# Kernel optimization log

Hardware: AMD Instinct MI355X
Metric: run time of the kernel (lower is better)

## Reference

```python
import jax, jax.numpy as jnp
import numpy as np

TAU = 0.07          # temperature
NEG = -1.0e9        # mask fill value (matches torch masked_fill)
EPS = 1e-12         # F.normalize eps

B1 = 4096
B2 = 4096
FDIM = 128


def setup_inputs() -> dict:
    key = jax.random.key(0)
    k1, k2 = jax.random.split(key)
    return {
        "feat_cls1": jax.random.normal(k1, (B1, FDIM), dtype=jnp.float32),
        "feat_cls2": jax.random.normal(k2, (B2, FDIM), dtype=jnp.float32),
    }


def reference(feat_cls1, feat_cls2):
    # concat both classes -> [B, F]
    feats = jnp.concatenate([feat_cls1, feat_cls2], axis=0)
    # F.normalize(dim=1): x / max(||x||, eps)
    norm = jnp.maximum(jnp.linalg.norm(feats, axis=1, keepdims=True), EPS)
    feats = feats / norm

    B = feats.shape[0]
    # similarity matrix [B, B]
    sim = (feats @ feats.T) / TAU

    labels = jnp.concatenate([
        jnp.zeros((feat_cls1.shape[0],), dtype=jnp.int32),
        jnp.ones((feat_cls2.shape[0],), dtype=jnp.int32),
    ])
    same_cls = labels[:, None] == labels[None, :]          # [B, B] bool
    eye = jnp.eye(B, dtype=bool)
    pool = same_cls & ~eye                                 # same-class, not self

    # select_mode == 'nearest': positive = same-class neighbor with max sim
    # (every row has >=1 same-class non-self entry since B1,B2 >= 2)
    pos_idx = jnp.argmax(jnp.where(pool, sim, NEG), axis=1)  # [B] int

    # allowed logits: all other-class entries + the single chosen positive; no diagonal
    pos_onehot = jax.nn.one_hot(pos_idx, B, dtype=bool)
    allow = (~same_cls) | pos_onehot
    allow = allow & ~eye

    sim_masked = jnp.where(allow, sim, NEG)
    # cross-entropy with target = pos_idx, mean over all B rows (all valid here)
    logz = jax.nn.logsumexp(sim_masked, axis=1)                              # [B]
    pos_logit = jnp.take_along_axis(sim_masked, pos_idx[:, None], axis=1)[:, 0]
    loss = jnp.mean(logz - pos_logit)
    return loss
```

## Files before the change

kernel.cpp:

```cpp
#include <hip/hip_runtime.h>
#include <math.h>
#include <stdint.h>

#define NB1   4096
#define NBTOT 8192
#define NFD   128
#define ECOLS 1024
#define BROWS 128
#define BCOLS 128
#define NTILES (ECOLS / BCOLS)

typedef __attribute__((ext_vector_type(8))) _Float16 f16x8;
typedef __attribute__((ext_vector_type(4))) float f32x4;
typedef _Float16 f16;

__device__ __forceinline__ void gl16(const f16* g, char* l) {
    __builtin_amdgcn_global_load_lds(
        (const __attribute__((address_space(1))) unsigned int*)g,
        (__attribute__((address_space(3))) unsigned int*)l,
        16, 0, 0);
}

__global__ void norm_k(const float* __restrict__ f1, const float* __restrict__ f2,
                       f16* __restrict__ nfh) {
    const int w = threadIdx.x >> 6, lane = threadIdx.x & 63;
    const int row = blockIdx.x * 4 + w;
    const float* src = (row < NB1) ? (f1 + (size_t)row * NFD)
                                   : (f2 + (size_t)(row - NB1) * NFD);
    const float2 v = *reinterpret_cast<const float2*>(src + 2 * lane);
    float s = v.x * v.x + v.y * v.y;
#pragma unroll
    for (int m = 32; m >= 1; m >>= 1) s += __shfl_xor(s, m, 64);
    const float inv = 1.0f / fmaxf(sqrtf(s), 1e-12f);
    const f16 h0 = (f16)(v.x * inv);
    const f16 h1 = (f16)(v.y * inv);
    const unsigned pack = (unsigned)__builtin_bit_cast(unsigned short, h0) |
                          ((unsigned)__builtin_bit_cast(unsigned short, h1) << 16);
    ((unsigned*)(nfh + (size_t)row * NFD))[lane] = pack;
}

__global__ __launch_bounds__(256, 2) void simstat_mfma(const f16* __restrict__ nfh,
                                                       float* __restrict__ posp,
                                                       float* __restrict__ sexpp) {
    extern __shared__ __align__(16) char smem[];

    const int e    = blockIdx.x;
    const int rt   = blockIdx.y;
    const int row0 = rt * BROWS;
    const int col0e = e * ECOLS;
    const bool same = ((row0 >= NB1) == (e >= 4));
    const int p = e & 3;

    const int t    = threadIdx.x;
    const int w    = t >> 6;
    const int lane = t & 63;
    const int lr   = lane & 15;
    const int lg   = lane >> 4;
    const int rowbase = 64 * (w >> 1);
    const int colbase = 64 * (w & 1);

    int goffs[8], dbase[8];
#pragma unroll
    for (int i = 0; i < 8; ++i) {
        const int base = w * 8192 + i * 1024;
        const int d    = base + lane * 16;
        const int sr   = d >> 8;
        const int slot = (d >> 4) & 15;
        const int kc   = slot ^ (sr & 15);
        goffs[i] = sr * NFD + kc * 8;
        dbase[i] = base;
    }
    int rbo[4], koff[4];
#pragma unroll
    for (int fb = 0; fb < 4; ++fb) rbo[fb] = (colbase + 16 * fb + lr) * 256;
#pragma unroll
    for (int ks = 0; ks < 4; ++ks) koff[ks] = (((ks << 2) + lg) ^ lr) << 4;

    {
        const f16* g0 = nfh + (size_t)col0e * NFD;
#pragma unroll
        for (int i = 0; i < 8; ++i) gl16(g0 + goffs[i], smem + dbase[i]);
    }

    f16x8 ah[4][4];
#pragma unroll
    for (int ks = 0; ks < 4; ++ks)
#pragma unroll
        for (int fa = 0; fa < 4; ++fa) {
            const size_t off = (size_t)(row0 + rowbase + 16 * fa + lr) * NFD + 32 * ks + 8 * lg;
            ah[ks][fa] = *reinterpret_cast<const f16x8*>(nfh + off);
        }

    __syncthreads();

    float stat[4][4];
#pragma unroll
    for (int fa = 0; fa < 4; ++fa)
#pragma unroll
        for (int r = 0; r < 4; ++r) stat[fa][r] = same ? -3.0e38f : 0.0f;
    const float K2 = 1.44269504089f / 0.07f;
    const float invtau = 1.0f / 0.07f;

#define LOADB(ks_, B_)                                                        \
    {                                                                         \
        _Pragma("unroll")                                                     \
        for (int fb = 0; fb < 4; ++fb)                                        \
            B_[fb] = *(const f16x8*)(bufB + rbo[fb] + koff[ks_]);             \
    }
#define MFMAS(ks_, B_)                                                        \
    {                                                                         \
        __builtin_amdgcn_s_setprio(1);                                        \
        _Pragma("unroll")                                                     \
        for (int fb = 0; fb < 4; ++fb)                                        \
            _Pragma("unroll")                                                 \
            for (int fa = 0; fa < 4; ++fa)                                    \
                acc[fa][fb] = __builtin_amdgcn_mfma_f32_16x16x32_f16(ah[ks_][fa], B_[fb], acc[fa][fb], 0, 0, 0); \
        __builtin_amdgcn_s_setprio(0);                                        \
    }

#pragma unroll 1
    for (int tile = 0; tile < NTILES; ++tile) {
        const char* bufB = smem + (tile & 1) * 32768;

        if (tile + 1 < NTILES) {
            char* nb = smem + ((tile + 1) & 1) * 32768;
            const f16* gn = nfh + (size_t)(col0e + (tile + 1) * BCOLS) * NFD;
#pragma unroll
            for (int i = 0; i < 8; ++i) gl16(gn + goffs[i], nb + dbase[i]);
        }

        f32x4 acc[4][4];
#pragma unroll
        for (int fa = 0; fa < 4; ++fa)
#pragma unroll
            for (int fb = 0; fb < 4; ++fb) {
                f32x4 z = {0.0f, 0.0f, 0.0f, 0.0f};
                acc[fa][fb] = z;
            }

        f16x8 b0[4], b1[4];
        LOADB(0, b0);
        LOADB(1, b1);
        MFMAS(0, b0);
        LOADB(2, b0);
        MFMAS(1, b1);
        LOADB(3, b1);
        MFMAS(2, b0);
        MFMAS(3, b1);

        if (same) {
            const int col0 = col0e + tile * BCOLS;
#pragma unroll
            for (int fa = 0; fa < 4; ++fa)
#pragma unroll
                for (int fb = 0; fb < 4; ++fb)
#pragma unroll
                    for (int r = 0; r < 4; ++r) {
                        const int grow = row0 + rowbase + 16 * fa + 4 * lg + r;
                        const int gcol = col0 + colbase + 16 * fb + lr;
                        stat[fa][r] = (grow == gcol) ? stat[fa][r]
                                                     : fmaxf(stat[fa][r], acc[fa][fb][r]);
                    }
        } else {
#pragma unroll
            for (int fa = 0; fa < 4; ++fa)
#pragma unroll
                for (int fb = 0; fb < 4; ++fb)
#pragma unroll
                    for (int r = 0; r < 4; ++r)
                        stat[fa][r] += exp2f(acc[fa][fb][r] * K2);
        }

        __syncthreads();
    }
#undef LOADB
#undef MFMAS

#pragma unroll
    for (int m = 1; m <= 8; m <<= 1) {
#pragma unroll
        for (int fa = 0; fa < 4; ++fa)
#pragma unroll
            for (int r = 0; r < 4; ++r) {
                const float o = __shfl_xor(stat[fa][r], m, 64);
                stat[fa][r] = same ? fmaxf(stat[fa][r], o) : (stat[fa][r] + o);
            }
    }

    float* scratch = (float*)smem;
    if (lr == 0) {
#pragma unroll
        for (int fa = 0; fa < 4; ++fa)
#pragma unroll
            for (int r = 0; r < 4; ++r) {
                const int rl = rowbase + 16 * fa + 4 * lg + r;
                scratch[(w & 1) * 128 + rl] = stat[fa][r];
            }
    }
    __syncthreads();
    if (t < 128) {
        const float v0 = scratch[t];
        const float v1 = scratch[128 + t];
        const float v = same ? fmaxf(v0, v1) * invtau : (v0 + v1);
        (same ? posp : sexpp)[(size_t)p * NBTOT + row0 + t] = v;
    }
}

__global__ void loss_part(const float* __restrict__ posp, const float* __restrict__ sexpp,
                          float* __restrict__ partial) {
    const int i = blockIdx.x * 256 + threadIdx.x;
    const float pv = fmaxf(fmaxf(posp[i], posp[NBTOT + i]),
                           fmaxf(posp[2 * NBTOT + i], posp[3 * NBTOT + i]));
    const float se = sexpp[i] + sexpp[NBTOT + i] + sexpp[2 * NBTOT + i] + sexpp[3 * NBTOT + i];
    float s = log1pf(se * __expf(-pv));
#pragma unroll
    for (int m = 32; m >= 1; m >>= 1) s += __shfl_xor(s, m, 64);
    __shared__ float part[4];
    if ((threadIdx.x & 63) == 0) part[threadIdx.x >> 6] = s;
    __syncthreads();
    if (threadIdx.x == 0)
        partial[blockIdx.x] = part[0] + part[1] + part[2] + part[3];
}

__global__ void loss_final(const float* __restrict__ partial, float* __restrict__ out) {
    const int t = threadIdx.x;
    float s = (t < 32) ? partial[t] : 0.0f;
#pragma unroll
    for (int m = 32; m >= 1; m >>= 1) s += __shfl_xor(s, m, 64);
    if (t == 0) out[0] = s / (float)NBTOT;
}

extern "C" void kernel_launch(void* const* d_in, const int* in_sizes, int n_in,
                              void* d_out, int out_size, void* d_ws, size_t ws_size,
                              hipStream_t stream) {
    const float* f1 = (const float*)d_in[0];
    const float* f2 = (const float*)d_in[1];

    f16*   nfh     = (f16*)d_ws;
    float* posp    = (float*)(nfh + (size_t)NBTOT * NFD);
    float* sexpp   = posp + 4 * NBTOT;
    float* partial = sexpp + 4 * NBTOT;

    (void)hipFuncSetAttribute(reinterpret_cast<const void*>(simstat_mfma),
                              hipFuncAttributeMaxDynamicSharedMemorySize, 65536);

    norm_k<<<NBTOT / 4, 256, 0, stream>>>(f1, f2, nfh);
    simstat_mfma<<<dim3(8, 64), 256, 65536, stream>>>(nfh, posp, sexpp);
    loss_part<<<NBTOT / 256, 256, 0, stream>>>(posp, sexpp, partial);
    loss_final<<<1, 64, 0, stream>>>(partial, (float*)d_out);
}
```

Measured before the change: 40.41 us.

## Fuse loss reduction into sim kernel and halve column tiles for occupancy

Splits the column range into 16 slices of 512 with 64-column tiles, which halves LDS use and allows three blocks per CU. The grid grows from 512 to 1024 blocks. The loss_part and loss_final kernels are removed and replaced by a last-block-done pattern inside the sim kernel, using atomic counters that norm_k zeroes. This removes two kernel launches and adds better latency hiding, at the cost of smaller MFMA tiles per B-load and the overhead of atomics and fences.

```diff
diff --git a/kernel.cpp b/kernel.cpp
--- a/kernel.cpp
+++ b/kernel.cpp
@@ -2,12 +2,13 @@
 #include <math.h>
 #include <stdint.h>
 
-#define NB1   4096
-#define NBTOT 8192
-#define NFD   128
-#define ECOLS 1024
-#define BROWS 128
-#define BCOLS 128
+#define NB1    4096
+#define NBTOT  8192
+#define NFD    128
+#define NSLICE 16
+#define ECOLS  512
+#define BROWS  128
+#define BCOLS  64
 #define NTILES (ECOLS / BCOLS)
 
 typedef __attribute__((ext_vector_type(8))) _Float16 f16x8;
@@ -22,7 +23,8 @@
 }
 
 __global__ void norm_k(const float* __restrict__ f1, const float* __restrict__ f2,
-                       f16* __restrict__ nfh) {
+                       f16* __restrict__ nfh, int* __restrict__ cnts) {
+    if (blockIdx.x == 0 && threadIdx.x < 65) cnts[threadIdx.x] = 0;
     const int w = threadIdx.x >> 6, lane = threadIdx.x & 63;
     const int row = blockIdx.x * 4 + w;
     const float* src = (row < NB1) ? (f1 + (size_t)row * NFD)
@@ -39,17 +41,21 @@
     ((unsigned*)(nfh + (size_t)row * NFD))[lane] = pack;
 }
 
-__global__ __launch_bounds__(256, 2) void simstat_mfma(const f16* __restrict__ nfh,
+__global__ __launch_bounds__(256, 3) void simstat_mfma(const f16* __restrict__ nfh,
                                                        float* __restrict__ posp,
-                                                       float* __restrict__ sexpp) {
+                                                       float* __restrict__ sexpp,
+                                                       int* __restrict__ rtcnt,
+                                                       int* __restrict__ gcnt,
+                                                       float* __restrict__ lossPartial,
+                                                       float* __restrict__ out) {
     extern __shared__ __align__(16) char smem[];
 
     const int e    = blockIdx.x;
     const int rt   = blockIdx.y;
     const int row0 = rt * BROWS;
     const int col0e = e * ECOLS;
-    const bool same = ((row0 >= NB1) == (e >= 4));
-    const int p = e & 3;
+    const bool same = ((row0 >= NB1) == (e >= 8));
+    const int p = e & 7;
 
     const int t    = threadIdx.x;
     const int w    = t >> 6;
@@ -57,12 +63,12 @@
     const int lr   = lane & 15;
     const int lg   = lane >> 4;
     const int rowbase = 64 * (w >> 1);
-    const int colbase = 64 * (w & 1);
-
-    int goffs[8], dbase[8];
-#pragma unroll
-    for (int i = 0; i < 8; ++i) {
-        const int base = w * 8192 + i * 1024;
+    const int colbase = 32 * (w & 1);
+
+    int goffs[4], dbase[4];
+#pragma unroll
+    for (int i = 0; i < 4; ++i) {
+        const int base = w * 4096 + i * 1024;
         const int d    = base + lane * 16;
         const int sr   = d >> 8;
         const int slot = (d >> 4) & 15;
@@ -70,16 +76,16 @@
         goffs[i] = sr * NFD + kc * 8;
         dbase[i] = base;
     }
-    int rbo[4], koff[4];
-#pragma unroll
-    for (int fb = 0; fb < 4; ++fb) rbo[fb] = (colbase + 16 * fb + lr) * 256;
+    int rbo[2], koff[4];
+#pragma unroll
+    for (int fb = 0; fb < 2; ++fb) rbo[fb] = (colbase + 16 * fb + lr) * 256;
 #pragma unroll
     for (int ks = 0; ks < 4; ++ks) koff[ks] = (((ks << 2) + lg) ^ lr) << 4;
 
     {
         const f16* g0 = nfh + (size_t)col0e * NFD;
 #pragma unroll
-        for (int i = 0; i < 8; ++i) gl16(g0 + goffs[i], smem + dbase[i]);
+        for (int i = 0; i < 4; ++i) gl16(g0 + goffs[i], smem + dbase[i]);
     }
 
     f16x8 ah[4][4];
@@ -101,59 +107,47 @@
     const float K2 = 1.44269504089f / 0.07f;
     const float invtau = 1.0f / 0.07f;
 
-#define LOADB(ks_, B_)                                                        \
-    {                                                                         \
-        _Pragma("unroll")                                                     \
-        for (int fb = 0; fb < 4; ++fb)                                        \
-            B_[fb] = *(const f16x8*)(bufB + rbo[fb] + koff[ks_]);             \
-    }
-#define MFMAS(ks_, B_)                                                        \
-    {                                                                         \
-        __builtin_amdgcn_s_setprio(1);                                        \
-        _Pragma("unroll")                                                     \
-        for (int fb = 0; fb < 4; ++fb)                                        \
-            _Pragma("unroll")                                                 \
-            for (int fa = 0; fa < 4; ++fa)                                    \
-                acc[fa][fb] = __builtin_amdgcn_mfma_f32_16x16x32_f16(ah[ks_][fa], B_[fb], acc[fa][fb], 0, 0, 0); \
-        __builtin_amdgcn_s_setprio(0);                                        \
-    }
-
 #pragma unroll 1
     for (int tile = 0; tile < NTILES; ++tile) {
-        const char* bufB = smem + (tile & 1) * 32768;
+        const char* bufB = smem + (tile & 1) * 16384;
 
         if (tile + 1 < NTILES) {
-            char* nb = smem + ((tile + 1) & 1) * 32768;
+            char* nb = smem + ((tile + 1) & 1) * 16384;
             const f16* gn = nfh + (size_t)(col0e + (tile + 1) * BCOLS) * NFD;
 #pragma unroll
-            for (int i = 0; i < 8; ++i) gl16(gn + goffs[i], nb + dbase[i]);
-        }
-
-        f32x4 acc[4][4];
+            for (int i = 0; i < 4; ++i) gl16(gn + goffs[i], nb + dbase[i]);
+        }
+
+        f32x4 acc[4][2];
 #pragma unroll
         for (int fa = 0; fa < 4; ++fa)
 #pragma unroll
-            for (int fb = 0; fb < 4; ++fb) {
+            for (int fb = 0; fb < 2; ++fb) {
                 f32x4 z = {0.0f, 0.0f, 0.0f, 0.0f};
                 acc[fa][fb] = z;
             }
 
-        f16x8 b0[4], b1[4];
-        LOADB(0, b0);
-        LOADB(1, b1);
-        MFMAS(0, b0);
-        LOADB(2, b0);
-        MFMAS(1, b1);
-        LOADB(3, b1);
-        MFMAS(2, b0);
-        MFMAS(3, b1);
+#pragma unroll
+        for (int ks = 0; ks < 4; ++ks) {
+            f16x8 b[2];
+#pragma unroll
+            for (int fb = 0; fb < 2; ++fb)
+                b[fb] = *(const f16x8*)(bufB + rbo[fb] + koff[ks]);
+            __builtin_amdgcn_s_setprio(1);
+#pragma unroll
+            for (int fb = 0; fb < 2; ++fb)
+#pragma unroll
+                for (int fa = 0; fa < 4; ++fa)
+                    acc[fa][fb] = __builtin_amdgcn_mfma_f32_16x16x32_f16(ah[ks][fa], b[fb], acc[fa][fb], 0, 0, 0);
+            __builtin_amdgcn_s_setprio(0);
+        }
 
         if (same) {
             const int col0 = col0e + tile * BCOLS;
 #pragma unroll
             for (int fa = 0; fa < 4; ++fa)
 #pragma unroll
-                for (int fb = 0; fb < 4; ++fb)
+                for (int fb = 0; fb < 2; ++fb)
 #pragma unroll
                     for (int r = 0; r < 4; ++r) {
                         const int grow = row0 + rowbase + 16 * fa + 4 * lg + r;
@@ -165,7 +159,7 @@
 #pragma unroll
             for (int fa = 0; fa < 4; ++fa)
 #pragma unroll
-                for (int fb = 0; fb < 4; ++fb)
+                for (int fb = 0; fb < 2; ++fb)
 #pragma unroll
                     for (int r = 0; r < 4; ++r)
                         stat[fa][r] += exp2f(acc[fa][fb][r] * K2);
@@ -173,8 +167,6 @@
 
         __syncthreads();
     }
-#undef LOADB
-#undef MFMAS
 
 #pragma unroll
     for (int m = 1; m <= 8; m <<= 1) {
@@ -204,30 +196,52 @@
         const float v = same ? fmaxf(v0, v1) * invtau : (v0 + v1);
         (same ? posp : sexpp)[(size_t)p * NBTOT + row0 + t] = v;
     }
-}
-
-__global__ void loss_part(const float* __restrict__ posp, const float* __restrict__ sexpp,
-                          float* __restrict__ partial) {
-    const int i = blockIdx.x * 256 + threadIdx.x;
-    const float pv = fmaxf(fmaxf(posp[i], posp[NBTOT + i]),
-                           fmaxf(posp[2 * NBTOT + i], posp[3 * NBTOT + i]));
-    const float se = sexpp[i] + sexpp[NBTOT + i] + sexpp[2 * NBTOT + i] + sexpp[3 * NBTOT + i];
-    float s = log1pf(se * __expf(-pv));
-#pragma unroll
-    for (int m = 32; m >= 1; m >>= 1) s += __shfl_xor(s, m, 64);
-    __shared__ float part[4];
-    if ((threadIdx.x & 63) == 0) part[threadIdx.x >> 6] = s;
-    __syncthreads();
-    if (threadIdx.x == 0)
-        partial[blockIdx.x] = part[0] + part[1] + part[2] + part[3];
-}
-
-__global__ void loss_final(const float* __restrict__ partial, float* __restrict__ out) {
-    const int t = threadIdx.x;
-    float s = (t < 32) ? partial[t] : 0.0f;
-#pragma unroll
-    for (int m = 32; m >= 1; m >>= 1) s += __shfl_xor(s, m, 64);
-    if (t == 0) out[0] = s / (float)NBTOT;
+    __syncthreads();
+
+    int* flags = (int*)smem;
+    if (t == 0) {
+        __threadfence();
+        const int old = atomicAdd(&rtcnt[rt], 1);
+        const int last = (old == NSLICE - 1);
+        if (last) __threadfence();
+        flags[0] = last;
+    }
+    __syncthreads();
+    if (!flags[0]) return;
+
+    float* scf = (float*)smem + 8;
+    float l = 0.0f;
+    if (t < 128) {
+        const int r = row0 + t;
+        float pv = -3.0e38f, se = 0.0f;
+#pragma unroll
+        for (int j = 0; j < 8; ++j) {
+            pv = fmaxf(pv, posp[(size_t)j * NBTOT + r]);
+            se += sexpp[(size_t)j * NBTOT + r];
+        }
+        l = log1pf(se * __expf(-pv));
+    }
+#pragma unroll
+    for (int m = 32; m >= 1; m >>= 1) l += __shfl_xor(l, m, 64);
+    if (t < 128 && lane == 0) scf[w] = l;
+    __syncthreads();
+    if (t == 0) {
+        lossPartial[rt] = scf[0] + scf[1];
+        __threadfence();
+        const int old = atomicAdd(gcnt, 1);
+        const int lastg = (old == 63);
+        if (lastg) __threadfence();
+        flags[1] = lastg;
+    }
+    __syncthreads();
+    if (!flags[1]) return;
+
+    if (t < 64) {
+        float s = lossPartial[t];
+#pragma unroll
+        for (int m = 32; m >= 1; m >>= 1) s += __shfl_xor(s, m, 64);
+        if (t == 0) out[0] = s / (float)NBTOT;
+    }
 }
 
 extern "C" void kernel_launch(void* const* d_in, const int* in_sizes, int n_in,
@@ -236,16 +250,16 @@
     const float* f1 = (const float*)d_in[0];
     const float* f2 = (const float*)d_in[1];
 
-    f16*   nfh     = (f16*)d_ws;
-    float* posp    = (float*)(nfh + (size_t)NBTOT * NFD);
-    float* sexpp   = posp + 4 * NBTOT;
-    float* partial = sexpp + 4 * NBTOT;
+    f16*   nfh         = (f16*)d_ws;
+    float* posp        = (float*)(nfh + (size_t)NBTOT * NFD);
+    float* sexpp       = posp + 8 * NBTOT;
+    float* lossPartial = sexpp + 8 * NBTOT;
+    int*   cnts        = (int*)(lossPartial + 64);
 
     (void)hipFuncSetAttribute(reinterpret_cast<const void*>(simstat_mfma),
-                              hipFuncAttributeMaxDynamicSharedMemorySize, 65536);
-
-    norm_k<<<NBTOT / 4, 256, 0, stream>>>(f1, f2, nfh);
-    simstat_mfma<<<dim3(8, 64), 256, 65536, stream>>>(nfh, posp, sexpp);
-    loss_part<<<NBTOT / 256, 256, 0, stream>>>(posp, sexpp, partial);
-    loss_final<<<1, 64, 0, stream>>>(partial, (float*)d_out);
-}
+                              hipFuncAttributeMaxDynamicSharedMemorySize, 32768);
+
+    norm_k<<<NBTOT / 4, 256, 0, stream>>>(f1, f2, nfh, cnts);
+    simstat_mfma<<<dim3(NSLICE, 64), 256, 32768, stream>>>(
+        nfh, posp, sexpp, cnts, cnts + 64, lossPartial, (float*)d_out);
+}
```

Result: slower. 65.17 us (+61.3%).

## Exploit symmetry of similarity matrix with upper-triangular tile blocks

Applied to the files above, without the earlier changes.

Replaces the full 8192x8192 tile sweep with one block per upper-triangular 128x128 tile pair (2080 blocks), so each tile's result feeds both row statistics and column statistics. This roughly halves MFMA and exp work, but each block now handles a single tile with no double-buffered pipelining. It also adds column reductions and expands the partial buffers to 32 slices, so loss_part reads 32 slices instead of 4.

```diff
diff --git a/kernel.cpp b/kernel.cpp
--- a/kernel.cpp
+++ b/kernel.cpp
@@ -2,13 +2,12 @@
 #include <math.h>
 #include <stdint.h>
 
-#define NB1   4096
-#define NBTOT 8192
-#define NFD   128
-#define ECOLS 1024
-#define BROWS 128
-#define BCOLS 128
-#define NTILES (ECOLS / BCOLS)
+#define NB1    4096
+#define NBTOT  8192
+#define NFD    128
+#define NT     64
+#define NPAIR  2080
+#define NSL    32
 
 typedef __attribute__((ext_vector_type(8))) _Float16 f16x8;
 typedef __attribute__((ext_vector_type(4))) float f32x4;
@@ -39,17 +38,21 @@
     ((unsigned*)(nfh + (size_t)row * NFD))[lane] = pack;
 }
 
-__global__ __launch_bounds__(256, 2) void simstat_mfma(const f16* __restrict__ nfh,
-                                                       float* __restrict__ posp,
-                                                       float* __restrict__ sexpp) {
-    extern __shared__ __align__(16) char smem[];
-
-    const int e    = blockIdx.x;
-    const int rt   = blockIdx.y;
-    const int row0 = rt * BROWS;
-    const int col0e = e * ECOLS;
-    const bool same = ((row0 >= NB1) == (e >= 4));
-    const int p = e & 3;
+__global__ __launch_bounds__(256, 2) void simstat_tri(const f16* __restrict__ nfh,
+                                                      float* __restrict__ posp,
+                                                      float* __restrict__ sexpp) {
+    __shared__ __align__(16) char smem[32768];
+
+    const int bid = blockIdx.x;
+    int rt = (int)((129.0 - sqrt(16641.0 - 8.0 * (double)bid)) * 0.5);
+    while ((rt + 1) * (129 - (rt + 1)) / 2 <= bid) ++rt;
+    while (rt * (129 - rt) / 2 > bid) --rt;
+    const int ct = rt + (bid - rt * (129 - rt) / 2);
+
+    const int row0 = rt * 128;
+    const int col0 = ct * 128;
+    const bool same = ((rt >= NSL) == (ct >= NSL));
+    const bool diag = (rt == ct);
 
     const int t    = threadIdx.x;
     const int w    = t >> 6;
@@ -59,28 +62,24 @@
     const int rowbase = 64 * (w >> 1);
     const int colbase = 64 * (w & 1);
 
-    int goffs[8], dbase[8];
-#pragma unroll
-    for (int i = 0; i < 8; ++i) {
-        const int base = w * 8192 + i * 1024;
-        const int d    = base + lane * 16;
-        const int sr   = d >> 8;
-        const int slot = (d >> 4) & 15;
-        const int kc   = slot ^ (sr & 15);
-        goffs[i] = sr * NFD + kc * 8;
-        dbase[i] = base;
-    }
+    {
+        const f16* g0 = nfh + (size_t)col0 * NFD;
+#pragma unroll
+        for (int i = 0; i < 8; ++i) {
+            const int base = w * 8192 + i * 1024;
+            const int d    = base + lane * 16;
+            const int sr   = d >> 8;
+            const int slot = (d >> 4) & 15;
+            const int kc   = slot ^ (sr & 15);
+            gl16(g0 + sr * NFD + kc * 8, smem + base);
+        }
+    }
+
     int rbo[4], koff[4];
 #pragma unroll
     for (int fb = 0; fb < 4; ++fb) rbo[fb] = (colbase + 16 * fb + lr) * 256;
 #pragma unroll
     for (int ks = 0; ks < 4; ++ks) koff[ks] = (((ks << 2) + lg) ^ lr) << 4;
-
-    {
-        const f16* g0 = nfh + (size_t)col0e * NFD;
-#pragma unroll
-        for (int i = 0; i < 8; ++i) gl16(g0 + goffs[i], smem + dbase[i]);
-    }
 
     f16x8 ah[4][4];
 #pragma unroll
@@ -93,19 +92,20 @@
 
     __syncthreads();
 
-    float stat[4][4];
+    f32x4 acc[4][4];
 #pragma unroll
     for (int fa = 0; fa < 4; ++fa)
 #pragma unroll
-        for (int r = 0; r < 4; ++r) stat[fa][r] = same ? -3.0e38f : 0.0f;
-    const float K2 = 1.44269504089f / 0.07f;
-    const float invtau = 1.0f / 0.07f;
+        for (int fb = 0; fb < 4; ++fb) {
+            f32x4 z = {0.0f, 0.0f, 0.0f, 0.0f};
+            acc[fa][fb] = z;
+        }
 
 #define LOADB(ks_, B_)                                                        \
     {                                                                         \
         _Pragma("unroll")                                                     \
         for (int fb = 0; fb < 4; ++fb)                                        \
-            B_[fb] = *(const f16x8*)(bufB + rbo[fb] + koff[ks_]);             \
+            B_[fb] = *(const f16x8*)(smem + rbo[fb] + koff[ks_]);             \
     }
 #define MFMAS(ks_, B_)                                                        \
     {                                                                         \
@@ -118,26 +118,7 @@
         __builtin_amdgcn_s_setprio(0);                                        \
     }
 
-#pragma unroll 1
-    for (int tile = 0; tile < NTILES; ++tile) {
-        const char* bufB = smem + (tile & 1) * 32768;
-
-        if (tile + 1 < NTILES) {
-            char* nb = smem + ((tile + 1) & 1) * 32768;
-            const f16* gn = nfh + (size_t)(col0e + (tile + 1) * BCOLS) * NFD;
-#pragma unroll
-            for (int i = 0; i < 8; ++i) gl16(gn + goffs[i], nb + dbase[i]);
-        }
-
-        f32x4 acc[4][4];
-#pragma unroll
-        for (int fa = 0; fa < 4; ++fa)
-#pragma unroll
-            for (int fb = 0; fb < 4; ++fb) {
-                f32x4 z = {0.0f, 0.0f, 0.0f, 0.0f};
-                acc[fa][fb] = z;
-            }
-
+    {
         f16x8 b0[4], b1[4];
         LOADB(0, b0);
         LOADB(1, b1);
@@ -147,76 +128,110 @@
         LOADB(3, b1);
         MFMAS(2, b0);
         MFMAS(3, b1);
-
-        if (same) {
-            const int col0 = col0e + tile * BCOLS;
-#pragma unroll
-            for (int fa = 0; fa < 4; ++fa)
-#pragma unroll
-                for (int fb = 0; fb < 4; ++fb)
-#pragma unroll
-                    for (int r = 0; r < 4; ++r) {
-                        const int grow = row0 + rowbase + 16 * fa + 4 * lg + r;
-                        const int gcol = col0 + colbase + 16 * fb + lr;
-                        stat[fa][r] = (grow == gcol) ? stat[fa][r]
-                                                     : fmaxf(stat[fa][r], acc[fa][fb][r]);
-                    }
-        } else {
-#pragma unroll
-            for (int fa = 0; fa < 4; ++fa)
-#pragma unroll
-                for (int fb = 0; fb < 4; ++fb)
-#pragma unroll
-                    for (int r = 0; r < 4; ++r)
-                        stat[fa][r] += exp2f(acc[fa][fb][r] * K2);
-        }
-
-        __syncthreads();
     }
 #undef LOADB
 #undef MFMAS
 
-#pragma unroll
-    for (int m = 1; m <= 8; m <<= 1) {
+    const float K2 = 1.44269504089f / 0.07f;
+    const float invtau = 1.0f / 0.07f;
+    float rstat[4][4];
+    float cstat[4];
+#pragma unroll
+    for (int fa = 0; fa < 4; ++fa)
+#pragma unroll
+        for (int r = 0; r < 4; ++r) rstat[fa][r] = same ? -3.0e38f : 0.0f;
+#pragma unroll
+    for (int fb = 0; fb < 4; ++fb) cstat[fb] = same ? -3.0e38f : 0.0f;
+
+    if (same) {
+#pragma unroll
+        for (int fa = 0; fa < 4; ++fa)
+#pragma unroll
+            for (int fb = 0; fb < 4; ++fb)
+#pragma unroll
+                for (int r = 0; r < 4; ++r) {
+                    const float v = acc[fa][fb][r];
+                    if (diag) {
+                        const int grow = rowbase + 16 * fa + 4 * lg + r;
+                        const int gcol = colbase + 16 * fb + lr;
+                        if (grow != gcol) rstat[fa][r] = fmaxf(rstat[fa][r], v);
+                    } else {
+                        rstat[fa][r] = fmaxf(rstat[fa][r], v);
+                        cstat[fb]    = fmaxf(cstat[fb], v);
+                    }
+                }
+    } else {
+#pragma unroll
+        for (int fa = 0; fa < 4; ++fa)
+#pragma unroll
+            for (int fb = 0; fb < 4; ++fb)
+#pragma unroll
+                for (int r = 0; r < 4; ++r) {
+                    const float e = exp2f(acc[fa][fb][r] * K2);
+                    rstat[fa][r] += e;
+                    cstat[fb]    += e;
+                }
+    }
+
+#pragma unroll
+    for (int m = 1; m <= 8; m <<= 1)
 #pragma unroll
         for (int fa = 0; fa < 4; ++fa)
 #pragma unroll
             for (int r = 0; r < 4; ++r) {
-                const float o = __shfl_xor(stat[fa][r], m, 64);
-                stat[fa][r] = same ? fmaxf(stat[fa][r], o) : (stat[fa][r] + o);
+                const float o = __shfl_xor(rstat[fa][r], m, 64);
+                rstat[fa][r] = same ? fmaxf(rstat[fa][r], o) : (rstat[fa][r] + o);
             }
-    }
-
-    float* scratch = (float*)smem;
+#pragma unroll
+    for (int m = 16; m <= 32; m <<= 1)
+#pragma unroll
+        for (int fb = 0; fb < 4; ++fb) {
+            const float o = __shfl_xor(cstat[fb], m, 64);
+            cstat[fb] = same ? fmaxf(cstat[fb], o) : (cstat[fb] + o);
+        }
+
+    __syncthreads();
+    float* scr = (float*)smem;
     if (lr == 0) {
 #pragma unroll
         for (int fa = 0; fa < 4; ++fa)
 #pragma unroll
-            for (int r = 0; r < 4; ++r) {
-                const int rl = rowbase + 16 * fa + 4 * lg + r;
-                scratch[(w & 1) * 128 + rl] = stat[fa][r];
-            }
-    }
-    __syncthreads();
+            for (int r = 0; r < 4; ++r)
+                scr[(w & 1) * 128 + rowbase + 16 * fa + 4 * lg + r] = rstat[fa][r];
+    }
+    if (lg == 0) {
+#pragma unroll
+        for (int fb = 0; fb < 4; ++fb)
+            scr[256 + (w >> 1) * 128 + colbase + 16 * fb + lr] = cstat[fb];
+    }
+    __syncthreads();
+
     if (t < 128) {
-        const float v0 = scratch[t];
-        const float v1 = scratch[128 + t];
-        const float v = same ? fmaxf(v0, v1) * invtau : (v0 + v1);
-        (same ? posp : sexpp)[(size_t)p * NBTOT + row0 + t] = v;
+        const float a = scr[t], b = scr[128 + t];
+        const float v = same ? fmaxf(a, b) * invtau : (a + b);
+        (same ? posp : sexpp)[(size_t)(ct & 31) * NBTOT + row0 + t] = v;
+    } else if (!diag) {
+        const int c = t - 128;
+        const float a = scr[256 + c], b = scr[384 + c];
+        const float v = same ? fmaxf(a, b) * invtau : (a + b);
+        (same ? posp : sexpp)[(size_t)(rt & 31) * NBTOT + col0 + c] = v;
     }
 }
 
 __global__ void loss_part(const float* __restrict__ posp, const float* __restrict__ sexpp,
                           float* __restrict__ partial) {
     const int i = blockIdx.x * 256 + threadIdx.x;
-    const float pv = fmaxf(fmaxf(posp[i], posp[NBTOT + i]),
-                           fmaxf(posp[2 * NBTOT + i], posp[3 * NBTOT + i]));
-    const float se = sexpp[i] + sexpp[NBTOT + i] + sexpp[2 * NBTOT + i] + sexpp[3 * NBTOT + i];
-    float s = log1pf(se * __expf(-pv));
-#pragma unroll
-    for (int m = 32; m >= 1; m >>= 1) s += __shfl_xor(s, m, 64);
+    float pv = -3.0e38f, se = 0.0f;
+#pragma unroll
+    for (int s = 0; s < NSL; ++s) {
+        pv = fmaxf(pv, posp[(size_t)s * NBTOT + i]);
+        se += sexpp[(size_t)s * NBTOT + i];
+    }
+    float l = log1pf(se * __expf(-pv));
+#pragma unroll
+    for (int m = 32; m >= 1; m >>= 1) l += __shfl_xor(l, m, 64);
     __shared__ float part[4];
-    if ((threadIdx.x & 63) == 0) part[threadIdx.x >> 6] = s;
+    if ((threadIdx.x & 63) == 0) part[threadIdx.x >> 6] = l;
     __syncthreads();
     if (threadIdx.x == 0)
         partial[blockIdx.x] = part[0] + part[1] + part[2] + part[3];
@@ -238,14 +253,11 @@
 
     f16*   nfh     = (f16*)d_ws;
     float* posp    = (float*)(nfh + (size_t)NBTOT * NFD);
-    float* sexpp   = posp + 4 * NBTOT;
-    float* partial = sexpp + 4 * NBTOT;
-
-    (void)hipFuncSetAttribute(reinterpret_cast<const void*>(simstat_mfma),
-                              hipFuncAttributeMaxDynamicSharedMemorySize, 65536);
+    float* sexpp   = posp + (size_t)NSL * NBTOT;
+    float* partial = sexpp + (size_t)NSL * NBTOT;
 
     norm_k<<<NBTOT / 4, 256, 0, stream>>>(f1, f2, nfh);
-    simstat_mfma<<<dim3(8, 64), 256, 65536, stream>>>(nfh, posp, sexpp);
+    simstat_tri<<<NPAIR, 256, 0, stream>>>(nfh, posp, sexpp);
     loss_part<<<NBTOT / 256, 256, 0, stream>>>(posp, sexpp, partial);
     loss_final<<<1, 64, 0, stream>>>(partial, (float*)d_out);
 }
```

New measurement: 55.09 us. +36.3%, slower.
